# Kernel optimization log

Measured on AMD Instinct MI355X. Metric: run time of the kernel, lower is better.

Reference implementation:

```python
import jax, jax.numpy as jnp
import numpy as np

N_HEAD = 16  # matches init_kwargs


def _rope_cos_sin(T, head_dim):
    # inv_freq over even indices, as in AdvancedRotaryEmbedding
    inv_freq = 1.0 / (10000.0 ** (jnp.arange(0, head_dim, 2, dtype=jnp.float32) / head_dim))
    t = jnp.arange(T, dtype=jnp.float32)
    freqs = t[:, None] * inv_freq[None, :]  # [T, head_dim/2]
    return jnp.cos(freqs), jnp.sin(freqs)


def _apply_rope(x, cos, sin):
    # x: [B, H, T, D]; cos/sin: [T, D/2] (broadcast over B, H)
    x1, x2 = x[..., 0::2], x[..., 1::2]
    # half-concat layout, faithful to the module's apply_rotary_emb
    return jnp.concatenate([x1 * cos - x2 * sin, x1 * sin + x2 * cos], axis=-1)


def reference(x, Wq, Wk, Wv, Wo):
    B, T, C = x.shape
    H = N_HEAD
    D = C // H
    # QKV projections (torch Linear: y = x @ W.T), then split heads -> [B, H, T, D]
    q = (x @ Wq.T).reshape(B, T, H, D).transpose(0, 2, 1, 3)
    k = (x @ Wk.T).reshape(B, T, H, D).transpose(0, 2, 1, 3)
    v = (x @ Wv.T).reshape(B, T, H, D).transpose(0, 2, 1, 3)
    cos, sin = _rope_cos_sin(T, D)
    cos = cos.astype(x.dtype)
    sin = sin.astype(x.dtype)
    q = _apply_rope(q, cos, sin)
    k = _apply_rope(k, cos, sin)
    # causal SDPA (eval mode -> dropout_p = 0); jax.nn expects [B, T, H, D]
    y = jax.nn.dot_product_attention(
        q.transpose(0, 2, 1, 3),
        k.transpose(0, 2, 1, 3),
        v.transpose(0, 2, 1, 3),
        is_causal=True,
    )  # [B, T, H, D]
    y = y.reshape(B, T, C)
    return y @ Wo.T


def setup_inputs() -> dict:
    key = jax.random.key(0)
    ks = jax.random.split(key, 5)
    B, T, C = 2, 2048, 1024
    s = 1.0 / np.sqrt(C)
    return {
        "x": jax.random.normal(ks[0], (B, T, C), dtype=jnp.float32),
        "Wq": jax.random.normal(ks[1], (C, C), dtype=jnp.float32) * s,
        "Wk": jax.random.normal(ks[2], (C, C), dtype=jnp.float32) * s,
        "Wv": jax.random.normal(ks[3], (C, C), dtype=jnp.float32) * s,
        "Wo": jax.random.normal(ks[4], (C, C), dtype=jnp.float32) * s,
    }
```

## Files before the change

kernel.cpp:

```cpp
#include <hip/hip_runtime.h>
#include <cstdint>
#include <cstddef>

typedef short s16x8 __attribute__((ext_vector_type(8)));
typedef float f32x4 __attribute__((ext_vector_type(4)));

#define MFMA16(a, b, c) __builtin_amdgcn_mfma_f32_16x16x32_bf16((a), (b), (c), 0, 0, 0)

constexpr int LDP = 72;
constexpr int LDW = 136;

__device__ __forceinline__ short f2bf(float f) {
    unsigned u = __builtin_bit_cast(unsigned, f);
    u += 0x7FFFu + ((u >> 16) & 1u);
    return (short)(u >> 16);
}
__device__ __forceinline__ float bf2f(short s) {
    unsigned u = ((unsigned)(unsigned short)s) << 16;
    return __builtin_bit_cast(float, u);
}
__device__ __forceinline__ unsigned pack2(float a, float b) {
    return (unsigned)(unsigned short)f2bf(a) | ((unsigned)(unsigned short)f2bf(b) << 16);
}
__device__ __forceinline__ unsigned pack2t(float a, float b) {
    unsigned ua = __builtin_bit_cast(unsigned, a);
    unsigned ub = __builtin_bit_cast(unsigned, b);
    return (ua >> 16) | (ub & 0xFFFF0000u);
}

__device__ __forceinline__ void async_ld16(const void* g, void* l) {
    __builtin_amdgcn_global_load_lds(
        (const __attribute__((address_space(1))) unsigned int*)g,
        (__attribute__((address_space(3))) unsigned int*)l, 16, 0, 0);
}

__global__ __launch_bounds__(256) void convert_kernel(
    const float* __restrict__ x, const float* __restrict__ Wq,
    const float* __restrict__ Wk, const float* __restrict__ Wv,
    const float* __restrict__ Wo, short* __restrict__ xb, short* __restrict__ wb) {
    const size_t f = ((size_t)blockIdx.x * 256 + threadIdx.x) * 8;
    const float* src;
    short* dst;
    if (f < 4194304) { src = x + f; dst = xb + f; }
    else {
        size_t wo = f - 4194304;
        int seg = (int)(wo >> 20);
        const float* ws4[4] = {Wq, Wk, Wv, Wo};
        src = ws4[seg] + (wo & 1048575u);
        dst = wb + wo;
    }
    float4 a = ((const float4*)src)[0];
    float4 b = ((const float4*)src)[1];
    *(uint4*)dst = make_uint4(pack2(a.x, a.y), pack2(a.z, a.w),
                              pack2(b.x, b.y), pack2(b.z, b.w));
}

__global__ __launch_bounds__(256) void qkv_kernel(
    const short* __restrict__ xb, const short* __restrict__ wb,
    short* __restrict__ Qo, short* __restrict__ Ko, short* __restrict__ VTo) {
    __shared__ __align__(16) short sA[128 * 64];
    __shared__ __align__(16) short sB[128 * 64];
    const int tid = threadIdx.x;
    const int w = tid >> 6, lane = tid & 63, quad = lane >> 4, l15 = lane & 15;
    const int wm = w & 1, wn = w >> 1;
    const int bx = blockIdx.x, by = blockIdx.y;
    const int m0 = by * 128;
    const int nb = bx * 128;

    f32x4 acc[4][4];
#pragma unroll
    for (int i = 0; i < 4; i++)
#pragma unroll
        for (int j = 0; j < 4; j++) acc[i][j] = f32x4{0.f, 0.f, 0.f, 0.f};

    for (int kb = 0; kb < 16; kb++) {
        const int k0 = kb * 64;
        if (kb) __syncthreads();
#pragma unroll
        for (int i = 0; i < 4; i++) {
            int c = i * 256 + tid;
            int row = c >> 3, col8 = (c & 7) * 8;
            async_ld16(xb + (size_t)(m0 + row) * 1024 + k0 + col8,
                       &sA[(i * 256 + w * 64) * 8]);
            async_ld16(wb + (size_t)(nb + row) * 1024 + k0 + col8,
                       &sB[(i * 256 + w * 64) * 8]);
        }
        __syncthreads();
#pragma unroll
        for (int ks = 0; ks < 2; ks++) {
            s16x8 av[4], bv[4];
#pragma unroll
            for (int at = 0; at < 4; at++)
                av[at] = *(const s16x8*)&sA[(wm * 64 + at * 16 + l15) * 64 + ks * 32 + quad * 8];
#pragma unroll
            for (int bt = 0; bt < 4; bt++)
                bv[bt] = *(const s16x8*)&sB[(wn * 64 + bt * 16 + l15) * 64 + ks * 32 + quad * 8];
#pragma unroll
            for (int at = 0; at < 4; at++)
#pragma unroll
                for (int bt = 0; bt < 4; bt++)
                    acc[at][bt] = MFMA16(av[at], bv[bt], acc[at][bt]);
        }
    }

    const int wsel = bx >> 3;
    const int h = (bx & 7) * 2 + wn;
    if (wsel == 2) {
#pragma unroll
        for (int at = 0; at < 4; at++) {
            int m = m0 + wm * 64 + at * 16 + quad * 4;
            int b = m >> 11, t0 = m & 2047;
            size_t base = ((size_t)((b * 16 + h) * 64)) * 2048;
#pragma unroll
            for (int bt = 0; bt < 4; bt++) {
                int d = bt * 16 + l15;
                unsigned lo = pack2(acc[at][bt][0], acc[at][bt][1]);
                unsigned hi = pack2(acc[at][bt][2], acc[at][bt][3]);
                *(uint2*)&VTo[base + (size_t)d * 2048 + t0] = make_uint2(lo, hi);
            }
        }
    } else {
        short* Out = (wsel == 0) ? Qo : Ko;
#pragma unroll
        for (int at = 0; at < 4; at++)
#pragma unroll
            for (int r = 0; r < 4; r++) {
                int m = m0 + wm * 64 + at * 16 + quad * 4 + r;
                int b = m >> 11, t = m & 2047;
                size_t base = (((size_t)(b * 16 + h)) * 2048 + t) * 64;
#pragma unroll
                for (int bt = 0; bt < 4; bt++)
                    Out[base + bt * 16 + l15] = f2bf(acc[at][bt][r]);
            }
    }
}

__global__ __launch_bounds__(256) void rope_kernel(short* __restrict__ Q, short* __restrict__ K) {
    const int rid = blockIdx.x * 256 + threadIdx.x;
    const bool isK = (rid & 65536) != 0;
    short* buf = isK ? K : Q;
    const float sc = isK ? 1.0f : 0.18033688011112042f;
    const int r2 = rid & 65535;
    const int t = r2 & 2047;
    short* row = buf + (size_t)r2 * 64;

    unsigned wv[32];
    const uint4* rp = (const uint4*)row;
#pragma unroll
    for (int c = 0; c < 8; c++) {
        uint4 v = rp[c];
        wv[c * 4 + 0] = v.x; wv[c * 4 + 1] = v.y; wv[c * 4 + 2] = v.z; wv[c * 4 + 3] = v.w;
    }
    float y1[32], y2[32];
    const float tf = (float)t;
#pragma unroll
    for (int i = 0; i < 32; i++) {
        float x1 = bf2f((short)(wv[i] & 0xFFFFu));
        float x2 = bf2f((short)(wv[i] >> 16));
        float inv = exp2f((float)i * -0.4152410118609203f);
        float rev = tf * inv * 0.15915494309189535f;
        rev = rev - floorf(rev);
        float sn = __builtin_amdgcn_sinf(rev);
        float cs = __builtin_amdgcn_cosf(rev);
        y1[i] = (x1 * cs - x2 * sn) * sc;
        y2[i] = (x1 * sn + x2 * cs) * sc;
    }
    unsigned ow[32];
#pragma unroll
    for (int i = 0; i < 16; i++) ow[i] = pack2(y1[2 * i], y1[2 * i + 1]);
#pragma unroll
    for (int i = 0; i < 16; i++) ow[16 + i] = pack2(y2[2 * i], y2[2 * i + 1]);
    uint4* wp = (uint4*)row;
#pragma unroll
    for (int c = 0; c < 8; c++)
        wp[c] = make_uint4(ow[c * 4 + 0], ow[c * 4 + 1], ow[c * 4 + 2], ow[c * 4 + 3]);
}

__global__ __launch_bounds__(256) void attn_kernel(
    const short* __restrict__ Q, const short* __restrict__ K,
    const short* __restrict__ VT, short* __restrict__ paO, float* __restrict__ ml) {
    __shared__ __align__(16) short sQP[64 * LDW];
    __shared__ __align__(16) short sK[128 * LDP];
    __shared__ __align__(16) short sVT[64 * LDW];

    const int tid = threadIdx.x;
    const int w = tid >> 6, lane = tid & 63, quad = lane >> 4, l15 = lane & 15;
    const int u = 79 - blockIdx.x;
    const int bh = blockIdx.y;

    int qt, c;
    if (u < 8)       { qt = u; c = 0; }
    else if (u < 24) { int v = u - 8;  qt = 8 + (v >> 1); c = v & 1; }
    else if (u < 48) { int v = u - 24; qt = 16 + v / 3;   c = v - 3 * (qt - 16); }
    else             { int v = u - 48; qt = 24 + (v >> 2); c = v & 3; }
    const int kbDiag = qt >> 1;
    const int kb0 = c * 4;
    const int kb1 = min(kb0 + 3, kbDiag);

    const short* Qp = Q + (size_t)bh * 2048 * 64;
    const short* Kp = K + (size_t)bh * 2048 * 64;
    const short* Vp = VT + (size_t)bh * 64 * 2048;

    const int krow = tid >> 3, kcol = (tid & 7) * 8;
    const int vrow = tid >> 4, vcol = (tid & 15) * 8;
    const short* Kld = Kp + (size_t)krow * 64 + kcol;
    const short* Vld = Vp + (size_t)vrow * 2048 + vcol;
    short* sKw = &sK[krow * LDP + kcol];
    short* sVw = &sVT[vrow * LDW + vcol];

    uint4 kr0, kr1, kr2, kr3, vr0, vr1, vr2, vr3;
#define LOADKV(KB) do {                                                  \
        const short* _kp = Kld + (size_t)(KB) * 8192;                    \
        kr0 = *(const uint4*)(_kp);                                      \
        kr1 = *(const uint4*)(_kp + 32 * 64);                            \
        kr2 = *(const uint4*)(_kp + 64 * 64);                            \
        kr3 = *(const uint4*)(_kp + 96 * 64);                            \
        const short* _vp = Vld + (KB) * 128;                             \
        vr0 = *(const uint4*)(_vp);                                      \
        vr1 = *(const uint4*)(_vp + 16 * 2048);                          \
        vr2 = *(const uint4*)(_vp + 32 * 2048);                          \
        vr3 = *(const uint4*)(_vp + 48 * 2048);                          \
    } while (0)

    uint4 qv0, qv1;
    {
        int p0 = tid, p1 = tid + 256;
        qv0 = *(const uint4*)(Qp + (size_t)(qt * 64 + (p0 >> 3)) * 64 + (p0 & 7) * 8);
        qv1 = *(const uint4*)(Qp + (size_t)(qt * 64 + (p1 >> 3)) * 64 + (p1 & 7) * 8);
        LOADKV(kb0);
        *(uint4*)&sQP[(p0 >> 3) * LDW + (p0 & 7) * 8] = qv0;
        *(uint4*)&sQP[(p1 >> 3) * LDW + (p1 & 7) * 8] = qv1;
    }
    __syncthreads();
    s16x8 aq[2];
#pragma unroll
    for (int ks = 0; ks < 2; ks++)
        aq[ks] = *(const s16x8*)&sQP[(w * 16 + l15) * LDW + ks * 32 + quad * 8];

    f32x4 o[4];
#pragma unroll
    for (int i = 0; i < 4; i++) o[i] = f32x4{0.f, 0.f, 0.f, 0.f};
    float lrun = 0.f;
    const int q_idx = qt * 64 + w * 16 + l15;

    for (int kb = kb0; kb <= kb1; kb++) {
        __syncthreads();
        *(uint4*)(sKw)            = kr0;
        *(uint4*)(sKw + 32 * LDP) = kr1;
        *(uint4*)(sKw + 64 * LDP) = kr2;
        *(uint4*)(sKw + 96 * LDP) = kr3;
        *(uint4*)(sVw)            = vr0;
        *(uint4*)(sVw + 16 * LDW) = vr1;
        *(uint4*)(sVw + 32 * LDW) = vr2;
        *(uint4*)(sVw + 48 * LDW) = vr3;
        __syncthreads();
        if (kb < kb1) LOADKV(kb + 1);

        f32x4 sa[8];
#pragma unroll
        for (int i = 0; i < 8; i++) sa[i] = f32x4{0.f, 0.f, 0.f, 0.f};
        __builtin_amdgcn_s_setprio(1);
#pragma unroll
        for (int ks = 0; ks < 2; ks++) {
#pragma unroll
            for (int ct = 0; ct < 8; ct++) {
                s16x8 kf = *(const s16x8*)&sK[(ct * 16 + l15) * LDP + ks * 32 + quad * 8];
                sa[ct] = MFMA16(kf, aq[ks], sa[ct]);
            }
        }
        __builtin_amdgcn_s_setprio(0);

        float ps[8][4];
#pragma unroll
        for (int ct = 0; ct < 8; ct++)
#pragma unroll
            for (int r = 0; r < 4; r++) ps[ct][r] = sa[ct][r];

        if (kb == kbDiag) {
#pragma unroll
            for (int ct = 0; ct < 8; ct++) {
                int kbase = kb * 128 + ct * 16 + quad * 4;
#pragma unroll
                for (int r = 0; r < 4; r++)
                    if ((kbase + r) > q_idx) ps[ct][r] = -INFINITY;
            }
        }

        float cm[8];
#pragma unroll
        for (int ct = 0; ct < 8; ct++) {
#pragma unroll
            for (int r = 0; r < 4; r++) ps[ct][r] = __builtin_amdgcn_exp2f(ps[ct][r]);
            cm[ct] = (ps[ct][0] + ps[ct][1]) + (ps[ct][2] + ps[ct][3]);
        }
        lrun += ((cm[0] + cm[1]) + (cm[2] + cm[3])) + ((cm[4] + cm[5]) + (cm[6] + cm[7]));

#pragma unroll
        for (int ct = 0; ct < 8; ct++) {
            unsigned lo = pack2t(ps[ct][0], ps[ct][1]);
            unsigned hi = pack2t(ps[ct][2], ps[ct][3]);
            *(uint2*)&sQP[(w * 16 + l15) * LDW + ct * 16 + quad * 4] = make_uint2(lo, hi);
        }

        __builtin_amdgcn_s_setprio(1);
#pragma unroll
        for (int ks2 = 0; ks2 < 4; ks2++) {
            s16x8 pa = *(const s16x8*)&sQP[(w * 16 + l15) * LDW + ks2 * 32 + quad * 8];
#pragma unroll
            for (int ct = 0; ct < 4; ct++) {
                s16x8 vb = *(const s16x8*)&sVT[(ct * 16 + l15) * LDW + ks2 * 32 + quad * 8];
                o[ct] = MFMA16(pa, vb, o[ct]);
            }
        }
        __builtin_amdgcn_s_setprio(0);
    }
#undef LOADKV

    const size_t pbase = ((size_t)(bh * 80 + u)) * 4096;
#pragma unroll
    for (int r = 0; r < 4; r++) {
        int row = w * 16 + quad * 4 + r;
#pragma unroll
        for (int ct = 0; ct < 4; ct++)
            paO[pbase + row * 64 + ct * 16 + l15] = f2bf(o[ct][r]);
    }
    lrun += __shfl_xor(lrun, 16);
    lrun += __shfl_xor(lrun, 32);
    if (quad == 0)
        ml[(bh * 80 + u) * 64 + w * 16 + l15] = lrun;
}

__global__ __launch_bounds__(256) void combine_kernel(
    const short* __restrict__ paO, const float* __restrict__ ml, short* __restrict__ Y) {
    const int qt = blockIdx.x, bh = blockIdx.y;
    const int b = bh >> 4, h = bh & 15;
    const int nch = (qt >> 3) + 1;
    int base;
    if (qt < 8) base = qt;
    else if (qt < 16) base = 8 + 2 * (qt - 8);
    else if (qt < 24) base = 24 + 3 * (qt - 16);
    else base = 48 + 4 * (qt - 24);

    const int row = threadIdx.x >> 2;
    const int cq = (threadIdx.x & 3) * 16;

    float L = 0.f;
    for (int i = 0; i < nch; i++)
        L += ml[(bh * 80 + base + i) * 64 + row];
    const float inv = 1.0f / L;

    float acc[16];
#pragma unroll
    for (int j = 0; j < 16; j++) acc[j] = 0.f;
    for (int i = 0; i < nch; i++) {
        const short* p = paO + ((size_t)(bh * 80 + base + i)) * 4096 + row * 64 + cq;
        uint4 v0 = ((const uint4*)p)[0];
        uint4 v1 = ((const uint4*)p)[1];
        unsigned vs[8] = {v0.x, v0.y, v0.z, v0.w, v1.x, v1.y, v1.z, v1.w};
#pragma unroll
        for (int j = 0; j < 8; j++) {
            acc[2 * j + 0] += bf2f((short)(vs[j] & 0xFFFFu));
            acc[2 * j + 1] += bf2f((short)(vs[j] >> 16));
        }
    }
    const int t = qt * 64 + row;
    short* yp = Y + ((size_t)(b * 2048 + t)) * 1024 + h * 64 + cq;
    unsigned ow[8];
#pragma unroll
    for (int j = 0; j < 8; j++) ow[j] = pack2(acc[2 * j] * inv, acc[2 * j + 1] * inv);
    ((uint4*)yp)[0] = make_uint4(ow[0], ow[1], ow[2], ow[3]);
    ((uint4*)yp)[1] = make_uint4(ow[4], ow[5], ow[6], ow[7]);
}

__global__ __launch_bounds__(256) void oproj_kernel(
    const short* __restrict__ Yb, const short* __restrict__ Wob, float* __restrict__ out) {
    __shared__ __align__(16) short sA[64 * 64];
    __shared__ __align__(16) short sB[128 * 64];
    const int tid = threadIdx.x;
    const int w = tid >> 6, lane = tid & 63, quad = lane >> 4, l15 = lane & 15;
    const int m0 = blockIdx.y * 64;
    const int nb = blockIdx.x * 128;

    f32x4 acc[4][2];
#pragma unroll
    for (int i = 0; i < 4; i++)
#pragma unroll
        for (int j = 0; j < 2; j++) acc[i][j] = f32x4{0.f, 0.f, 0.f, 0.f};

    for (int kb = 0; kb < 16; kb++) {
        const int k0 = kb * 64;
        if (kb) __syncthreads();
#pragma unroll
        for (int i = 0; i < 2; i++) {
            int c = i * 256 + tid;
            int row = c >> 3, col8 = (c & 7) * 8;
            async_ld16(Yb + (size_t)(m0 + row) * 1024 + k0 + col8,
                       &sA[(i * 256 + w * 64) * 8]);
        }
#pragma unroll
        for (int i = 0; i < 4; i++) {
            int c = i * 256 + tid;
            int row = c >> 3, col8 = (c & 7) * 8;
            async_ld16(Wob + (size_t)(nb + row) * 1024 + k0 + col8,
                       &sB[(i * 256 + w * 64) * 8]);
        }
        __syncthreads();
#pragma unroll
        for (int ks = 0; ks < 2; ks++) {
            s16x8 av[4], bv[2];
#pragma unroll
            for (int at = 0; at < 4; at++)
                av[at] = *(const s16x8*)&sA[(at * 16 + l15) * 64 + ks * 32 + quad * 8];
#pragma unroll
            for (int bt = 0; bt < 2; bt++)
                bv[bt] = *(const s16x8*)&sB[(w * 32 + bt * 16 + l15) * 64 + ks * 32 + quad * 8];
#pragma unroll
            for (int at = 0; at < 4; at++)
#pragma unroll
                for (int bt = 0; bt < 2; bt++)
                    acc[at][bt] = MFMA16(av[at], bv[bt], acc[at][bt]);
        }
    }
#pragma unroll
    for (int at = 0; at < 4; at++)
#pragma unroll
        for (int r = 0; r < 4; r++) {
            int m = m0 + at * 16 + quad * 4 + r;
#pragma unroll
            for (int bt = 0; bt < 2; bt++) {
                int n = nb + w * 32 + bt * 16 + l15;
                out[(size_t)m * 1024 + n] = acc[at][bt][r];
            }
        }
}

extern "C" void kernel_launch(void* const* d_in, const int* in_sizes, int n_in,
                              void* d_out, int out_size, void* d_ws, size_t ws_size,
                              hipStream_t stream) {
    (void)in_sizes; (void)n_in; (void)out_size; (void)ws_size;
    const float* x  = (const float*)d_in[0];
    const float* Wq = (const float*)d_in[1];
    const float* Wk = (const float*)d_in[2];
    const float* Wv = (const float*)d_in[3];
    const float* Wo = (const float*)d_in[4];
    float* out = (float*)d_out;

    const size_t NE = (size_t)2 * 16 * 2048 * 64;
    short* Q   = (short*)d_ws;
    short* K   = Q + NE;
    short* VT  = K + NE;
    short* Y   = VT + NE;
    short* xb  = Y;
    short* wb  = Y + NE;
    short* paO = wb + NE;
    float* ml  = (float*)(paO + (size_t)32 * 80 * 4096);

    convert_kernel<<<4096, 256, 0, stream>>>(x, Wq, Wk, Wv, Wo, xb, wb);
    qkv_kernel<<<dim3(24, 32), 256, 0, stream>>>(xb, wb, Q, K, VT);
    rope_kernel<<<512, 256, 0, stream>>>(Q, K);
    attn_kernel<<<dim3(80, 32), 256, 0, stream>>>(Q, K, VT, paO, ml);
    combine_kernel<<<dim3(32, 32), 256, 0, stream>>>(paO, ml, Y);
    oproj_kernel<<<dim3(8, 64), 256, 0, stream>>>(Y, wb + 3 * 1048576, out);
}
```

Baseline: 197.1 us.

## Rebalance attention work split into 8-block KV chunks with new schedule

The causal attention split grows from 4 to 8 key blocks per work item, so each query tile has at most two partial chunks. The grid shrinks from 80 to 48 blocks per head, with a hand-built ordering that issues the longest chunks first. The combine kernel changes to merge at most two partials, which cuts partial-output traffic. Q fragments now load straight from global memory into registers instead of going through shared memory and a barrier. The cost is fewer blocks per launch and longer serial loops per block.

```diff
diff --git a/kernel.cpp b/kernel.cpp
--- a/kernel.cpp
+++ b/kernel.cpp
@@ -185,17 +185,20 @@
 
     const int tid = threadIdx.x;
     const int w = tid >> 6, lane = tid & 63, quad = lane >> 4, l15 = lane & 15;
-    const int u = 79 - blockIdx.x;
+    const int s = blockIdx.x;
     const int bh = blockIdx.y;
 
     int qt, c;
-    if (u < 8)       { qt = u; c = 0; }
-    else if (u < 24) { int v = u - 8;  qt = 8 + (v >> 1); c = v & 1; }
-    else if (u < 48) { int v = u - 24; qt = 16 + v / 3;   c = v - 3 * (qt - 16); }
-    else             { int v = u - 48; qt = 24 + (v >> 2); c = v & 3; }
+    if (s < 18)      { qt = 14 + s; c = 0; }
+    else if (s < 20) { qt = 30 + (s - 18); c = 1; }
+    else {
+        int v = s - 20, L = v >> 2, j = v & 3;
+        if (j < 2) { qt = 12 - 2 * L + j; c = 0; }
+        else       { qt = 28 - 2 * L + (j - 2); c = 1; }
+    }
     const int kbDiag = qt >> 1;
-    const int kb0 = c * 4;
-    const int kb1 = min(kb0 + 3, kbDiag);
+    const int kb0 = c * 8;
+    const int kb1 = min(kb0 + 7, kbDiag);
 
     const short* Qp = Q + (size_t)bh * 2048 * 64;
     const short* Kp = K + (size_t)bh * 2048 * 64;
@@ -222,20 +225,11 @@
         vr3 = *(const uint4*)(_vp + 48 * 2048);                          \
     } while (0)
 
-    uint4 qv0, qv1;
-    {
-        int p0 = tid, p1 = tid + 256;
-        qv0 = *(const uint4*)(Qp + (size_t)(qt * 64 + (p0 >> 3)) * 64 + (p0 & 7) * 8);
-        qv1 = *(const uint4*)(Qp + (size_t)(qt * 64 + (p1 >> 3)) * 64 + (p1 & 7) * 8);
-        LOADKV(kb0);
-        *(uint4*)&sQP[(p0 >> 3) * LDW + (p0 & 7) * 8] = qv0;
-        *(uint4*)&sQP[(p1 >> 3) * LDW + (p1 & 7) * 8] = qv1;
-    }
-    __syncthreads();
     s16x8 aq[2];
 #pragma unroll
     for (int ks = 0; ks < 2; ks++)
-        aq[ks] = *(const s16x8*)&sQP[(w * 16 + l15) * LDW + ks * 32 + quad * 8];
+        aq[ks] = *(const s16x8*)(Qp + (size_t)(qt * 64 + w * 16 + l15) * 64 + ks * 32 + quad * 8);
+    LOADKV(kb0);
 
     f32x4 o[4];
 #pragma unroll
@@ -316,7 +310,7 @@
     }
 #undef LOADKV
 
-    const size_t pbase = ((size_t)(bh * 80 + u)) * 4096;
+    const size_t pbase = ((size_t)(bh * 48 + s)) * 4096;
 #pragma unroll
     for (int r = 0; r < 4; r++) {
         int row = w * 16 + quad * 4 + r;
@@ -327,33 +321,34 @@
     lrun += __shfl_xor(lrun, 16);
     lrun += __shfl_xor(lrun, 32);
     if (quad == 0)
-        ml[(bh * 80 + u) * 64 + w * 16 + l15] = lrun;
+        ml[(bh * 48 + s) * 64 + w * 16 + l15] = lrun;
 }
 
 __global__ __launch_bounds__(256) void combine_kernel(
     const short* __restrict__ paO, const float* __restrict__ ml, short* __restrict__ Y) {
     const int qt = blockIdx.x, bh = blockIdx.y;
     const int b = bh >> 4, h = bh & 15;
-    const int nch = (qt >> 3) + 1;
-    int base;
-    if (qt < 8) base = qt;
-    else if (qt < 16) base = 8 + 2 * (qt - 8);
-    else if (qt < 24) base = 24 + 3 * (qt - 16);
-    else base = 48 + 4 * (qt - 24);
+
+    int u0, u1 = -1;
+    if (qt >= 14) u0 = qt - 14;
+    else          u0 = 20 + 4 * ((13 - qt) >> 1) + (qt & 1);
+    if (qt >= 30)      u1 = 18 + (qt - 30);
+    else if (qt >= 16) u1 = 22 + 4 * ((29 - qt) >> 1) + (qt & 1);
 
     const int row = threadIdx.x >> 2;
     const int cq = (threadIdx.x & 3) * 16;
 
-    float L = 0.f;
-    for (int i = 0; i < nch; i++)
-        L += ml[(bh * 80 + base + i) * 64 + row];
+    float L = ml[(bh * 48 + u0) * 64 + row];
+    if (u1 >= 0) L += ml[(bh * 48 + u1) * 64 + row];
     const float inv = 1.0f / L;
 
     float acc[16];
 #pragma unroll
     for (int j = 0; j < 16; j++) acc[j] = 0.f;
-    for (int i = 0; i < nch; i++) {
-        const short* p = paO + ((size_t)(bh * 80 + base + i)) * 4096 + row * 64 + cq;
+    for (int i = 0; i < 2; i++) {
+        int uu = i ? u1 : u0;
+        if (uu < 0) break;
+        const short* p = paO + ((size_t)(bh * 48 + uu)) * 4096 + row * 64 + cq;
         uint4 v0 = ((const uint4*)p)[0];
         uint4 v1 = ((const uint4*)p)[1];
         unsigned vs[8] = {v0.x, v0.y, v0.z, v0.w, v1.x, v1.y, v1.z, v1.w};
@@ -453,12 +448,12 @@
     short* xb  = Y;
     short* wb  = Y + NE;
     short* paO = wb + NE;
-    float* ml  = (float*)(paO + (size_t)32 * 80 * 4096);
+    float* ml  = (float*)(paO + (size_t)32 * 48 * 4096);
 
     convert_kernel<<<4096, 256, 0, stream>>>(x, Wq, Wk, Wv, Wo, xb, wb);
     qkv_kernel<<<dim3(24, 32), 256, 0, stream>>>(xb, wb, Q, K, VT);
     rope_kernel<<<512, 256, 0, stream>>>(Q, K);
-    attn_kernel<<<dim3(80, 32), 256, 0, stream>>>(Q, K, VT, paO, ml);
+    attn_kernel<<<dim3(48, 32), 256, 0, stream>>>(Q, K, VT, paO, ml);
     combine_kernel<<<dim3(32, 32), 256, 0, stream>>>(paO, ml, Y);
     oproj_kernel<<<dim3(8, 64), 256, 0, stream>>>(Y, wb + 3 * 1048576, out);
 }
```

Measured after the change: 197.6 us. No clear change (+0.3%).
